# Kernel optimization log

Hardware: AMD Instinct MI355X
Metric: run time of the kernel (lower is better)

Reference implementation:

```python
import jax, jax.numpy as jnp
import numpy as np


def setup_inputs() -> dict:
    key = jax.random.key(0)
    k1, k2 = jax.random.split(key)
    B, N = 4096, 2048
    mid = jax.random.normal(k1, (B, N), dtype=jnp.float32)
    half = jax.random.uniform(k2, (B, N), dtype=jnp.float32) * 0.5
    l = mid - half  # lower bound
    u = mid + half  # upper bound (l <= u elementwise)
    return {"l": l, "u": u}


def reference(l, u):
    # Original torch code builds (B, n, n) tensors: for the lower bound, row i is
    # u[b, :] with entry i replaced by l[b, i]; it softmaxes each row and extracts
    # the diagonal. Diagonal of that softmax equals:
    #   lower[b, i] = exp(l[b,i]) / (exp(l[b,i]) + sum_{j != i} exp(u[b,j]))
    # and symmetrically for the upper bound. Softmax is shift-invariant, so we
    # stabilize with a per-row global max M and use the sum-exclude-one trick,
    # computing the exact same math in O(B*n) instead of O(B*n^2).
    M = jnp.maximum(jnp.max(l, axis=-1, keepdims=True),
                    jnp.max(u, axis=-1, keepdims=True))  # (B, 1)
    e_l = jnp.exp(l - M)  # (B, n)
    e_u = jnp.exp(u - M)  # (B, n)
    S_l = jnp.sum(e_l, axis=-1, keepdims=True)  # (B, 1)
    S_u = jnp.sum(e_u, axis=-1, keepdims=True)  # (B, 1)
    lower_result = e_l / (e_l + (S_u - e_u))  # diag of softmax(lower rows)
    upper_result = e_u / (e_u + (S_l - e_l))  # diag of softmax(upper rows)
    return lower_result, upper_result
```

## Files before the change

kernel.cpp:

```cpp
#include <hip/hip_runtime.h>

#define NCOL 2048
#define VEC_PER_ROW (NCOL / 4)
#define PER_LANE 8
#define BLOCK 256

typedef float f32x4 __attribute__((ext_vector_type(4)));

__device__ __forceinline__ float waveReduceMax(float v) {
#pragma unroll
    for (int o = 32; o > 0; o >>= 1) v = fmaxf(v, __shfl_xor(v, o, 64));
    return v;
}
__device__ __forceinline__ float waveReduceSum(float v) {
#pragma unroll
    for (int o = 32; o > 0; o >>= 1) v += __shfl_xor(v, o, 64);
    return v;
}

__global__ __launch_bounds__(BLOCK) void interval_softmax_kernel(
    const float* __restrict__ L, const float* __restrict__ U,
    float* __restrict__ lo, float* __restrict__ up)
{
    const int wave = threadIdx.x >> 6;
    const int lane = threadIdx.x & 63;
    const int row  = blockIdx.x * (BLOCK / 64) + wave;

    const f32x4* L4 = reinterpret_cast<const f32x4*>(L) + (size_t)row * VEC_PER_ROW;
    const f32x4* U4 = reinterpret_cast<const f32x4*>(U) + (size_t)row * VEC_PER_ROW;

    f32x4 a[PER_LANE], b[PER_LANE];
#pragma unroll
    for (int k = 0; k < PER_LANE; ++k) a[k] = L4[lane + 64 * k];
#pragma unroll
    for (int k = 0; k < PER_LANE; ++k) b[k] = U4[lane + 64 * k];

    float m = -3.402823466e38f;
#pragma unroll
    for (int k = 0; k < PER_LANE; ++k) {
        m = fmaxf(m, fmaxf(fmaxf(a[k].x, a[k].y), fmaxf(a[k].z, a[k].w)));
        m = fmaxf(m, fmaxf(fmaxf(b[k].x, b[k].y), fmaxf(b[k].z, b[k].w)));
    }
    m = waveReduceMax(m);

    float sl = 0.f, su = 0.f;
#pragma unroll
    for (int k = 0; k < PER_LANE; ++k) {
        a[k].x = __expf(a[k].x - m); a[k].y = __expf(a[k].y - m);
        a[k].z = __expf(a[k].z - m); a[k].w = __expf(a[k].w - m);
        b[k].x = __expf(b[k].x - m); b[k].y = __expf(b[k].y - m);
        b[k].z = __expf(b[k].z - m); b[k].w = __expf(b[k].w - m);
        sl += (a[k].x + a[k].y) + (a[k].z + a[k].w);
        su += (b[k].x + b[k].y) + (b[k].z + b[k].w);
    }
    sl = waveReduceSum(sl);
    su = waveReduceSum(su);

    f32x4* lo4 = reinterpret_cast<f32x4*>(lo) + (size_t)row * VEC_PER_ROW;
    f32x4* up4 = reinterpret_cast<f32x4*>(up) + (size_t)row * VEC_PER_ROW;
#pragma unroll
    for (int k = 0; k < PER_LANE; ++k) {
        f32x4 o, p;
        o.x = __fdividef(a[k].x, a[k].x + (su - b[k].x));
        o.y = __fdividef(a[k].y, a[k].y + (su - b[k].y));
        o.z = __fdividef(a[k].z, a[k].z + (su - b[k].z));
        o.w = __fdividef(a[k].w, a[k].w + (su - b[k].w));
        p.x = __fdividef(b[k].x, b[k].x + (sl - a[k].x));
        p.y = __fdividef(b[k].y, b[k].y + (sl - a[k].y));
        p.z = __fdividef(b[k].z, b[k].z + (sl - a[k].z));
        p.w = __fdividef(b[k].w, b[k].w + (sl - a[k].w));
        __builtin_nontemporal_store(o, &lo4[lane + 64 * k]);
        __builtin_nontemporal_store(p, &up4[lane + 64 * k]);
    }
}

extern "C" void kernel_launch(void* const* d_in, const int* in_sizes, int n_in,
                              void* d_out, int out_size, void* d_ws, size_t ws_size,
                              hipStream_t stream) {
    const float* L = (const float*)d_in[0];
    const float* U = (const float*)d_in[1];
    const int rows = in_sizes[0] / NCOL;
    float* lo = (float*)d_out;
    float* up = lo + (size_t)rows * NCOL;
    const int rows_per_block = BLOCK / 64;
    interval_softmax_kernel<<<rows / rows_per_block, BLOCK, 0, stream>>>(L, U, lo, up);
}
```

Before: 25.65 us.

## Split fused softmax into row-statistics pass and elementwise ratio pass

Replaces the single fused kernel with two kernels. The first computes per-row max and exp sums into workspace. The second re-reads L and U elementwise, recomputes the exponentials and writes the ratios. This lowers register pressure and improves parallelism in the output pass, but adds a second full read of both inputs and an extra launch.

```diff
diff --git a/kernel.cpp b/kernel.cpp
--- a/kernel.cpp
+++ b/kernel.cpp
@@ -2,8 +2,9 @@
 
 #define NCOL 2048
 #define VEC_PER_ROW (NCOL / 4)
-#define PER_LANE 8
-#define BLOCK 256
+#define P1_PER_LANE 8
+#define P1_BLOCK 256
+#define P2_BLOCK 256
 
 typedef float f32x4 __attribute__((ext_vector_type(4)));
 
@@ -18,26 +19,26 @@
     return v;
 }
 
-__global__ __launch_bounds__(BLOCK) void interval_softmax_kernel(
+__global__ __launch_bounds__(P1_BLOCK) void stats_kernel(
     const float* __restrict__ L, const float* __restrict__ U,
-    float* __restrict__ lo, float* __restrict__ up)
+    f32x4* __restrict__ stats)
 {
     const int wave = threadIdx.x >> 6;
     const int lane = threadIdx.x & 63;
-    const int row  = blockIdx.x * (BLOCK / 64) + wave;
+    const int row  = blockIdx.x * (P1_BLOCK / 64) + wave;
 
     const f32x4* L4 = reinterpret_cast<const f32x4*>(L) + (size_t)row * VEC_PER_ROW;
     const f32x4* U4 = reinterpret_cast<const f32x4*>(U) + (size_t)row * VEC_PER_ROW;
 
-    f32x4 a[PER_LANE], b[PER_LANE];
+    f32x4 a[P1_PER_LANE], b[P1_PER_LANE];
 #pragma unroll
-    for (int k = 0; k < PER_LANE; ++k) a[k] = L4[lane + 64 * k];
+    for (int k = 0; k < P1_PER_LANE; ++k) a[k] = L4[lane + 64 * k];
 #pragma unroll
-    for (int k = 0; k < PER_LANE; ++k) b[k] = U4[lane + 64 * k];
+    for (int k = 0; k < P1_PER_LANE; ++k) b[k] = U4[lane + 64 * k];
 
     float m = -3.402823466e38f;
 #pragma unroll
-    for (int k = 0; k < PER_LANE; ++k) {
+    for (int k = 0; k < P1_PER_LANE; ++k) {
         m = fmaxf(m, fmaxf(fmaxf(a[k].x, a[k].y), fmaxf(a[k].z, a[k].w)));
         m = fmaxf(m, fmaxf(fmaxf(b[k].x, b[k].y), fmaxf(b[k].z, b[k].w)));
     }
@@ -45,33 +46,53 @@
 
     float sl = 0.f, su = 0.f;
 #pragma unroll
-    for (int k = 0; k < PER_LANE; ++k) {
-        a[k].x = __expf(a[k].x - m); a[k].y = __expf(a[k].y - m);
-        a[k].z = __expf(a[k].z - m); a[k].w = __expf(a[k].w - m);
-        b[k].x = __expf(b[k].x - m); b[k].y = __expf(b[k].y - m);
-        b[k].z = __expf(b[k].z - m); b[k].w = __expf(b[k].w - m);
-        sl += (a[k].x + a[k].y) + (a[k].z + a[k].w);
-        su += (b[k].x + b[k].y) + (b[k].z + b[k].w);
+    for (int k = 0; k < P1_PER_LANE; ++k) {
+        sl += (__expf(a[k].x - m) + __expf(a[k].y - m))
+            + (__expf(a[k].z - m) + __expf(a[k].w - m));
+        su += (__expf(b[k].x - m) + __expf(b[k].y - m))
+            + (__expf(b[k].z - m) + __expf(b[k].w - m));
     }
     sl = waveReduceSum(sl);
     su = waveReduceSum(su);
 
-    f32x4* lo4 = reinterpret_cast<f32x4*>(lo) + (size_t)row * VEC_PER_ROW;
-    f32x4* up4 = reinterpret_cast<f32x4*>(up) + (size_t)row * VEC_PER_ROW;
-#pragma unroll
-    for (int k = 0; k < PER_LANE; ++k) {
-        f32x4 o, p;
-        o.x = __fdividef(a[k].x, a[k].x + (su - b[k].x));
-        o.y = __fdividef(a[k].y, a[k].y + (su - b[k].y));
-        o.z = __fdividef(a[k].z, a[k].z + (su - b[k].z));
-        o.w = __fdividef(a[k].w, a[k].w + (su - b[k].w));
-        p.x = __fdividef(b[k].x, b[k].x + (sl - a[k].x));
-        p.y = __fdividef(b[k].y, b[k].y + (sl - a[k].y));
-        p.z = __fdividef(b[k].z, b[k].z + (sl - a[k].z));
-        p.w = __fdividef(b[k].w, b[k].w + (sl - a[k].w));
-        __builtin_nontemporal_store(o, &lo4[lane + 64 * k]);
-        __builtin_nontemporal_store(p, &up4[lane + 64 * k]);
+    if (lane == 0) {
+        f32x4 s; s.x = m; s.y = sl; s.z = su; s.w = 0.f;
+        stats[row] = s;
     }
+}
+
+__global__ __launch_bounds__(P2_BLOCK) void ratio_kernel(
+    const float* __restrict__ L, const float* __restrict__ U,
+    const f32x4* __restrict__ stats,
+    float* __restrict__ lo, float* __restrict__ up)
+{
+    const size_t v   = (size_t)blockIdx.x * P2_BLOCK + threadIdx.x;
+    const int    row = (int)(v >> 9);
+
+    const f32x4 s = stats[row];
+    const float m = s.x, sl = s.y, su = s.z;
+
+    const f32x4 a = reinterpret_cast<const f32x4*>(L)[v];
+    const f32x4 b = reinterpret_cast<const f32x4*>(U)[v];
+
+    f32x4 el, eu;
+    el.x = __expf(a.x - m); el.y = __expf(a.y - m);
+    el.z = __expf(a.z - m); el.w = __expf(a.w - m);
+    eu.x = __expf(b.x - m); eu.y = __expf(b.y - m);
+    eu.z = __expf(b.z - m); eu.w = __expf(b.w - m);
+
+    f32x4 o, p;
+    o.x = __fdividef(el.x, el.x + (su - eu.x));
+    o.y = __fdividef(el.y, el.y + (su - eu.y));
+    o.z = __fdividef(el.z, el.z + (su - eu.z));
+    o.w = __fdividef(el.w, el.w + (su - eu.w));
+    p.x = __fdividef(eu.x, eu.x + (sl - el.x));
+    p.y = __fdividef(eu.y, eu.y + (sl - el.y));
+    p.z = __fdividef(eu.z, eu.z + (sl - el.z));
+    p.w = __fdividef(eu.w, eu.w + (sl - el.w));
+
+    __builtin_nontemporal_store(o, &reinterpret_cast<f32x4*>(lo)[v]);
+    __builtin_nontemporal_store(p, &reinterpret_cast<f32x4*>(up)[v]);
 }
 
 extern "C" void kernel_launch(void* const* d_in, const int* in_sizes, int n_in,
@@ -82,6 +103,12 @@
     const int rows = in_sizes[0] / NCOL;
     float* lo = (float*)d_out;
     float* up = lo + (size_t)rows * NCOL;
-    const int rows_per_block = BLOCK / 64;
-    interval_softmax_kernel<<<rows / rows_per_block, BLOCK, 0, stream>>>(L, U, lo, up);
+    f32x4* stats = (f32x4*)d_ws;
+
+    const int p1_blocks = rows / (P1_BLOCK / 64);
+    stats_kernel<<<p1_blocks, P1_BLOCK, 0, stream>>>(L, U, stats);
+
+    const int total_vec = rows * VEC_PER_ROW;
+    const int p2_blocks = total_vec / P2_BLOCK;
+    ratio_kernel<<<p2_blocks, P2_BLOCK, 0, stream>>>(L, U, stats, lo, up);
 }
```

New measurement: 36.17 us. +41.0%, slower.
